# Kernel optimization log

Measured on AMD Instinct MI355X. Metric: run time of the kernel, lower is better.

The kernel has to match this reference:

```python
import jax, jax.numpy as jnp
import numpy as np

IN_FEATURES = 16384
OUT_FEATURES = 16384
NNZ = 1_000_000
BATCH = 256


def setup_inputs() -> dict:
    key = jax.random.key(0)
    k_x, k_w, k_b, k_r, k_c = jax.random.split(key, 5)
    x = jax.random.normal(k_x, (BATCH, IN_FEATURES), dtype=jnp.float32)
    weight_vals = jax.random.normal(k_w, (NNZ,), dtype=jnp.float32)
    bias = jax.random.normal(k_b, (OUT_FEATURES,), dtype=jnp.float32)
    rows = jax.random.randint(k_r, (NNZ,), 0, OUT_FEATURES, dtype=jnp.int32)
    cols = jax.random.randint(k_c, (NNZ,), 0, IN_FEATURES, dtype=jnp.int32)
    return {"x": x, "weight_vals": weight_vals, "bias": bias,
            "rows": rows, "cols": cols}


def reference(x, weight_vals, bias, rows, cols):
    # SparseLinear forward: y = x @ W^T + b, with W sparse COO of shape
    # [out_features, in_features]; (rows, cols) are W's nnz coordinates.
    # Per-edge contribution: x[:, col] * W[row, col], scattered into out[:, row].
    contrib = x[:, cols] * weight_vals  # [B, nnz]
    # segment-sum edges into output features: [nnz, B] -> [out, B]
    out = jax.ops.segment_sum(contrib.T, rows, num_segments=OUT_FEATURES).T
    return out + bias  # [B, out_features]
```

## Files before the change

### kernel.cpp

```cpp
#include <hip/hip_runtime.h>
#include <hip/hip_bf16.h>
#include <hip/hip_fp16.h>

#define BATCH_N 256
#define IN_F    16384
#define OUT_F   16384
#define CAP     128
#define NBUCK   512
#define CAPB    2560
#define EPB     2048
#define TBLK    1024

typedef unsigned int u32x4 __attribute__((ext_vector_type(4)));
typedef float f32x4 __attribute__((ext_vector_type(4)));


__global__ void prep_kernel(const float* __restrict__ x,
                            __hip_bfloat16* __restrict__ xTh,
                            const int* __restrict__ rows,
                            const int* __restrict__ cols,
                            const float* __restrict__ vals, int nnz,
                            int* __restrict__ gcursor,
                            uint2* __restrict__ staging) {
    __shared__ int smem[64 * 65];
    int t = threadIdx.x;
    if (blockIdx.x < TBLK) {
        float* tile = (float*)smem;
        int bid = blockIdx.x;
        int i0 = (bid & 255) * 64;
        int b0 = (bid >> 8) * 64;
        int tx4 = t & 15;
        int r16 = t >> 4;
#pragma unroll
        for (int k = 0; k < 4; ++k) {
            int row = r16 + k * 16;
            f32x4 v = *(const f32x4*)(x + (size_t)(b0 + row) * IN_F + i0 + tx4 * 4);
            tile[row * 65 + tx4 * 4 + 0] = v.x;
            tile[row * 65 + tx4 * 4 + 1] = v.y;
            tile[row * 65 + tx4 * 4 + 2] = v.z;
            tile[row * 65 + tx4 * 4 + 3] = v.w;
        }
        __syncthreads();
        int tx = t & 63, ty = t >> 6;
        int h = b0 >> 7, j0 = b0 & 127;
#pragma unroll
        for (int k = 0; k < 64; k += 4) {
            int col = i0 + ty + k;
            xTh[((size_t)h * IN_F + col) * 128 + j0 + tx] =
                __float2bfloat16(tile[tx * 65 + ty + k]);
        }
    } else {
        int* hist = smem;
        int* base = smem + NBUCK;
        hist[t] = 0; hist[t + 256] = 0;
        __syncthreads();
        int i0 = (blockIdx.x - TBLK) * EPB;
        unsigned int pack[8], vb[8];
        int bk[8];
#pragma unroll
        for (int k = 0; k < 8; ++k) {
            int i = i0 + k * 256 + t;
            if (i < nnz) {
                int r = rows[i], c = cols[i];
                pack[k] = ((unsigned int)r << 14) | (unsigned int)c;
                vb[k] = __float_as_uint(vals[i]);
                bk[k] = r >> 5;
                atomicAdd(&hist[bk[k]], 1);
            } else bk[k] = -1;
        }
        __syncthreads();
#pragma unroll
        for (int q = 0; q < 2; ++q) {
            int bin = t + q * 256;
            int h = hist[bin];
            base[bin] = (h > 0) ? atomicAdd(&gcursor[bin], h) : 0;
        }
        __syncthreads();
        hist[t] = 0; hist[t + 256] = 0;
        __syncthreads();
#pragma unroll
        for (int k = 0; k < 8; ++k) {
            if (bk[k] >= 0) {
                int p = base[bk[k]] + atomicAdd(&hist[bk[k]], 1);
                if (p < CAPB)
                    staging[(size_t)bk[k] * CAPB + p] = make_uint2(pack[k], vb[k]);
            }
        }
    }
}


__global__ void __launch_bounds__(512)
bucket_scatter_kernel(const uint2* __restrict__ staging,
                      const int* __restrict__ gcursor,
                      unsigned int* __restrict__ edges,
                      int* __restrict__ counts) {
    __shared__ int lcnt[32];
    __shared__ unsigned int lbin[32 * CAP];
    int b = blockIdx.x;
    int t = threadIdx.x;
    if (t < 32) lcnt[t] = 0;
    __syncthreads();
    int n = gcursor[b];
    if (n > CAPB) n = CAPB;
    const uint2* st = staging + (size_t)b * CAPB;
    for (int i = t; i < n; i += 512) {
        uint2 rec = __builtin_nontemporal_load((const unsigned long long*)st + i)
                        ? make_uint2(0, 0) : make_uint2(0, 0);
        (void)rec;
        uint2 r2;
        {
            unsigned long long v =
                __builtin_nontemporal_load((const unsigned long long*)st + i);
            r2.x = (unsigned int)(v & 0xffffffffull);
            r2.y = (unsigned int)(v >> 32);
        }
        int rl = (r2.x >> 14) & 31;
        int p = atomicAdd(&lcnt[rl], 1);
        if (p < CAP) {
            unsigned int col = r2.x & 16383u;
            __half hv = __float2half(__uint_as_float(r2.y));
            lbin[rl * CAP + p] = (col << 16) | (unsigned int)__half_as_ushort(hv);
        }
    }
    __syncthreads();
    if (t < 32) {
        int c = lcnt[t];
        if (c > CAP) c = CAP;
        counts[b * 32 + t] = (c + 7) & ~7;
    }
    unsigned int* dst = edges + (size_t)b * 32 * CAP;
    for (int i4 = t; i4 < 32 * CAP / 4; i4 += 512) {
        int i = i4 * 4;
        int row = i >> 7;
        int slot = i & (CAP - 1);
        int c = lcnt[row];
        if (c > CAP) c = CAP;
        int lim = (c + 7) & ~7;
        if (slot < lim) {
            u32x4 v;
            v.x = (slot + 0 < c) ? lbin[i + 0] : 0u;
            v.y = (slot + 1 < c) ? lbin[i + 1] : 0u;
            v.z = (slot + 2 < c) ? lbin[i + 2] : 0u;
            v.w = (slot + 3 < c) ? lbin[i + 3] : 0u;
            __builtin_nontemporal_store(v, (u32x4*)(dst + i));
        }
    }
}


__global__ void accum_kernel(const unsigned int* __restrict__ xh0,
                             const unsigned int* __restrict__ edges,
                             const int*   __restrict__ counts,
                             const float* __restrict__ bias,
                             float* __restrict__ out) {
    __shared__ float slab[128][17];
    int blk = blockIdx.x;
    int h = blk & 1;
    int o0 = (blk >> 1) * 16;
    int w = threadIdx.x >> 6;
    int lane = threadIdx.x & 63;
    const unsigned int* xh = xh0 + (size_t)h * IN_F * 64;
#pragma unroll
    for (int rr = 0; rr < 4; ++rr) {
        int rl = w * 4 + rr;
        int o = __builtin_amdgcn_readfirstlane(o0 + rl);
        int n = counts[o];
        const u32x4* el4 = (const u32x4*)(edges + (size_t)o * CAP);
        float ax = 0.f, ay = 0.f;
        u32x4 ca = el4[0], cb = el4[1];
        for (int j = 0; j < n; j += 8) {
            u32x4 na = el4[(j >> 2) + 2];
            u32x4 nb = el4[(j >> 2) + 3];
            unsigned int e[8];
            e[0] = ca.x; e[1] = ca.y; e[2] = ca.z; e[3] = ca.w;
            e[4] = cb.x; e[5] = cb.y; e[6] = cb.z; e[7] = cb.w;
            unsigned int g[8];
#pragma unroll
            for (int k = 0; k < 8; ++k) {
                const unsigned int* p = xh + ((e[k] >> 16) << 6);
                g[k] = p[lane];
            }
#pragma unroll
            for (int k = 0; k < 8; ++k) {
                float v = __half2float(__ushort_as_half((unsigned short)(e[k] & 0xffffu)));
                ax += __uint_as_float(g[k] << 16) * v;
                ay += __uint_as_float(g[k] & 0xffff0000u) * v;
            }
            ca = na; cb = nb;
        }
        float bv = bias[o];
        slab[2 * lane + 0][rl] = ax + bv;
        slab[2 * lane + 1][rl] = ay + bv;
    }
    __syncthreads();
#pragma unroll
    for (int it = 0; it < 2; ++it) {
        int item = threadIdx.x + it * 256;
        int bl = item >> 2;
        int q = item & 3;
        f32x4 v;
        v.x = slab[bl][q * 4 + 0];
        v.y = slab[bl][q * 4 + 1];
        v.z = slab[bl][q * 4 + 2];
        v.w = slab[bl][q * 4 + 3];
        __builtin_nontemporal_store(v,
            (f32x4*)(out + (size_t)(h * 128 + bl) * OUT_F + o0 + q * 4));
    }
}

extern "C" void kernel_launch(void* const* d_in, const int* in_sizes, int n_in,
                              void* d_out, int out_size, void* d_ws, size_t ws_size,
                              hipStream_t stream) {
    const float* x     = (const float*)d_in[0];
    const float* wvals = (const float*)d_in[1];
    const float* bias  = (const float*)d_in[2];
    const int*   rows  = (const int*)d_in[3];
    const int*   cols  = (const int*)d_in[4];
    float* out = (float*)d_out;
    int nnz = in_sizes[1];

    const size_t MB = 1024 * 1024;
    char* ws = (char*)d_ws;
    __hip_bfloat16* xTh = (__hip_bfloat16*)(ws);
    uint2* staging = (uint2*)(ws + 8 * MB);
    unsigned int* edges = (unsigned int*)(ws + 22 * MB);
    int*   gcursor = (int*)(ws + 30 * MB);
    int*   counts  = (int*)(ws + 30 * MB + 4096);

    (void)hipMemsetAsync(gcursor, 0, NBUCK * sizeof(int), stream);

    int npart = (nnz + EPB - 1) / EPB;
    prep_kernel<<<TBLK + npart, 256, 0, stream>>>(x, xTh, rows, cols, wvals, nnz,
                                                  gcursor, staging);
    bucket_scatter_kernel<<<NBUCK, 512, 0, stream>>>(staging, gcursor, edges, counts);
    accum_kernel<<<(OUT_F / 16) * 2, 256, 0, stream>>>((const unsigned int*)xTh, edges,
                                                       counts, bias, out);
}
```

Before: 141.2 us.

## Scatter edges directly into per-XCD row buckets and drop bucket-scatter kernel

Replaces the two-pass histogram/staging plus bucket-scatter pipeline with a direct per-edge global atomic into per-row cursors. The cursors are partitioned by the XCC ID read from a hardware register, so atomics stay within one die's L2 and do not contend across XCDs. Each record is packed to fp16 value plus column and written straight into a fixed 32-slot sub-bucket per row per XCD. The accumulation kernel then walks the 8 sub-buckets per row. This removes one kernel launch and the staging round trip, but needs a 17 MB memset to zero the padding and adds inner-loop overhead across 8 small sub-lists.

```diff
diff --git a/kernel.cpp b/kernel.cpp
--- a/kernel.cpp
+++ b/kernel.cpp
@@ -5,14 +5,19 @@
 #define BATCH_N 256
 #define IN_F    16384
 #define OUT_F   16384
-#define CAP     128
-#define NBUCK   512
-#define CAPB    2560
+#define NXCD    8
+#define CAPX    32
 #define EPB     2048
 #define TBLK    1024
 
 typedef unsigned int u32x4 __attribute__((ext_vector_type(4)));
 typedef float f32x4 __attribute__((ext_vector_type(4)));
+
+__device__ inline int get_xcc() {
+    unsigned int x;
+    asm volatile("s_getreg_b32 %0, hwreg(HW_REG_XCC_ID)" : "=s"(x));
+    return (int)(x & 7);
+}
 
 
 __global__ void prep_kernel(const float* __restrict__ x,
@@ -20,12 +25,11 @@
                             const int* __restrict__ rows,
                             const int* __restrict__ cols,
                             const float* __restrict__ vals, int nnz,
-                            int* __restrict__ gcursor,
-                            uint2* __restrict__ staging) {
-    __shared__ int smem[64 * 65];
+                            int* __restrict__ cursor,
+                            unsigned int* __restrict__ edges) {
+    __shared__ float tile[64 * 65];
     int t = threadIdx.x;
     if (blockIdx.x < TBLK) {
-        float* tile = (float*)smem;
         int bid = blockIdx.x;
         int i0 = (bid & 255) * 64;
         int b0 = (bid >> 8) * 64;
@@ -50,100 +54,21 @@
                 __float2bfloat16(tile[tx * 65 + ty + k]);
         }
     } else {
-        int* hist = smem;
-        int* base = smem + NBUCK;
-        hist[t] = 0; hist[t + 256] = 0;
-        __syncthreads();
+        int sub = get_xcc();
+        int* cur = cursor + sub * OUT_F;
         int i0 = (blockIdx.x - TBLK) * EPB;
-        unsigned int pack[8], vb[8];
-        int bk[8];
 #pragma unroll
         for (int k = 0; k < 8; ++k) {
             int i = i0 + k * 256 + t;
             if (i < nnz) {
-                int r = rows[i], c = cols[i];
-                pack[k] = ((unsigned int)r << 14) | (unsigned int)c;
-                vb[k] = __float_as_uint(vals[i]);
-                bk[k] = r >> 5;
-                atomicAdd(&hist[bk[k]], 1);
-            } else bk[k] = -1;
-        }
-        __syncthreads();
-#pragma unroll
-        for (int q = 0; q < 2; ++q) {
-            int bin = t + q * 256;
-            int h = hist[bin];
-            base[bin] = (h > 0) ? atomicAdd(&gcursor[bin], h) : 0;
-        }
-        __syncthreads();
-        hist[t] = 0; hist[t + 256] = 0;
-        __syncthreads();
-#pragma unroll
-        for (int k = 0; k < 8; ++k) {
-            if (bk[k] >= 0) {
-                int p = base[bk[k]] + atomicAdd(&hist[bk[k]], 1);
-                if (p < CAPB)
-                    staging[(size_t)bk[k] * CAPB + p] = make_uint2(pack[k], vb[k]);
+                int r = rows[i];
+                unsigned int c = (unsigned int)cols[i];
+                __half hv = __float2half(vals[i]);
+                unsigned int rec = (c << 16) | (unsigned int)__half_as_ushort(hv);
+                int pos = atomicAdd(&cur[r], 1);
+                if (pos < CAPX)
+                    edges[((size_t)r * NXCD + sub) * CAPX + pos] = rec;
             }
-        }
-    }
-}
-
-
-__global__ void __launch_bounds__(512)
-bucket_scatter_kernel(const uint2* __restrict__ staging,
-                      const int* __restrict__ gcursor,
-                      unsigned int* __restrict__ edges,
-                      int* __restrict__ counts) {
-    __shared__ int lcnt[32];
-    __shared__ unsigned int lbin[32 * CAP];
-    int b = blockIdx.x;
-    int t = threadIdx.x;
-    if (t < 32) lcnt[t] = 0;
-    __syncthreads();
-    int n = gcursor[b];
-    if (n > CAPB) n = CAPB;
-    const uint2* st = staging + (size_t)b * CAPB;
-    for (int i = t; i < n; i += 512) {
-        uint2 rec = __builtin_nontemporal_load((const unsigned long long*)st + i)
-                        ? make_uint2(0, 0) : make_uint2(0, 0);
-        (void)rec;
-        uint2 r2;
-        {
-            unsigned long long v =
-                __builtin_nontemporal_load((const unsigned long long*)st + i);
-            r2.x = (unsigned int)(v & 0xffffffffull);
-            r2.y = (unsigned int)(v >> 32);
-        }
-        int rl = (r2.x >> 14) & 31;
-        int p = atomicAdd(&lcnt[rl], 1);
-        if (p < CAP) {
-            unsigned int col = r2.x & 16383u;
-            __half hv = __float2half(__uint_as_float(r2.y));
-            lbin[rl * CAP + p] = (col << 16) | (unsigned int)__half_as_ushort(hv);
-        }
-    }
-    __syncthreads();
-    if (t < 32) {
-        int c = lcnt[t];
-        if (c > CAP) c = CAP;
-        counts[b * 32 + t] = (c + 7) & ~7;
-    }
-    unsigned int* dst = edges + (size_t)b * 32 * CAP;
-    for (int i4 = t; i4 < 32 * CAP / 4; i4 += 512) {
-        int i = i4 * 4;
-        int row = i >> 7;
-        int slot = i & (CAP - 1);
-        int c = lcnt[row];
-        if (c > CAP) c = CAP;
-        int lim = (c + 7) & ~7;
-        if (slot < lim) {
-            u32x4 v;
-            v.x = (slot + 0 < c) ? lbin[i + 0] : 0u;
-            v.y = (slot + 1 < c) ? lbin[i + 1] : 0u;
-            v.z = (slot + 2 < c) ? lbin[i + 2] : 0u;
-            v.w = (slot + 3 < c) ? lbin[i + 3] : 0u;
-            __builtin_nontemporal_store(v, (u32x4*)(dst + i));
         }
     }
 }
@@ -151,7 +76,7 @@
 
 __global__ void accum_kernel(const unsigned int* __restrict__ xh0,
                              const unsigned int* __restrict__ edges,
-                             const int*   __restrict__ counts,
+                             const int*   __restrict__ cursor,
                              const float* __restrict__ bias,
                              float* __restrict__ out) {
     __shared__ float slab[128][17];
@@ -165,29 +90,29 @@
     for (int rr = 0; rr < 4; ++rr) {
         int rl = w * 4 + rr;
         int o = __builtin_amdgcn_readfirstlane(o0 + rl);
-        int n = counts[o];
-        const u32x4* el4 = (const u32x4*)(edges + (size_t)o * CAP);
+        const unsigned int* re = edges + (size_t)o * (NXCD * CAPX);
         float ax = 0.f, ay = 0.f;
-        u32x4 ca = el4[0], cb = el4[1];
-        for (int j = 0; j < n; j += 8) {
-            u32x4 na = el4[(j >> 2) + 2];
-            u32x4 nb = el4[(j >> 2) + 3];
-            unsigned int e[8];
-            e[0] = ca.x; e[1] = ca.y; e[2] = ca.z; e[3] = ca.w;
-            e[4] = cb.x; e[5] = cb.y; e[6] = cb.z; e[7] = cb.w;
-            unsigned int g[8];
+        for (int sub = 0; sub < NXCD; ++sub) {
+            int n = cursor[sub * OUT_F + o];
+            if (n > CAPX) n = CAPX;
+            const unsigned int* el = re + sub * CAPX;
+            for (int j = 0; j < n; j += 8) {
+                unsigned int e[8];
 #pragma unroll
-            for (int k = 0; k < 8; ++k) {
-                const unsigned int* p = xh + ((e[k] >> 16) << 6);
-                g[k] = p[lane];
+                for (int k = 0; k < 8; ++k) e[k] = el[j + k];
+                unsigned int g[8];
+#pragma unroll
+                for (int k = 0; k < 8; ++k) {
+                    const unsigned int* p = xh + ((e[k] >> 16) << 6);
+                    g[k] = p[lane];
+                }
+#pragma unroll
+                for (int k = 0; k < 8; ++k) {
+                    float v = __half2float(__ushort_as_half((unsigned short)(e[k] & 0xffffu)));
+                    ax += __uint_as_float(g[k] << 16) * v;
+                    ay += __uint_as_float(g[k] & 0xffff0000u) * v;
+                }
             }
-#pragma unroll
-            for (int k = 0; k < 8; ++k) {
-                float v = __half2float(__ushort_as_half((unsigned short)(e[k] & 0xffffu)));
-                ax += __uint_as_float(g[k] << 16) * v;
-                ay += __uint_as_float(g[k] & 0xffff0000u) * v;
-            }
-            ca = na; cb = nb;
         }
         float bv = bias[o];
         slab[2 * lane + 0][rl] = ax + bv;
@@ -223,17 +148,14 @@
     const size_t MB = 1024 * 1024;
     char* ws = (char*)d_ws;
     __hip_bfloat16* xTh = (__hip_bfloat16*)(ws);
-    uint2* staging = (uint2*)(ws + 8 * MB);
-    unsigned int* edges = (unsigned int*)(ws + 22 * MB);
-    int*   gcursor = (int*)(ws + 30 * MB);
-    int*   counts  = (int*)(ws + 30 * MB + 4096);
+    int* cursor = (int*)(ws + 8 * MB);
+    unsigned int* edges = (unsigned int*)(ws + 9 * MB);
 
-    (void)hipMemsetAsync(gcursor, 0, NBUCK * sizeof(int), stream);
+    (void)hipMemsetAsync(ws + 8 * MB, 0, 17 * MB, stream);
 
     int npart = (nnz + EPB - 1) / EPB;
     prep_kernel<<<TBLK + npart, 256, 0, stream>>>(x, xTh, rows, cols, wvals, nnz,
-                                                  gcursor, staging);
-    bucket_scatter_kernel<<<NBUCK, 512, 0, stream>>>(staging, gcursor, edges, counts);
+                                                  cursor, edges);
     accum_kernel<<<(OUT_F / 16) * 2, 256, 0, stream>>>((const unsigned int*)xTh, edges,
-                                                       counts, bias, out);
+                                                       cursor, bias, out);
 }
```

Result: slower. 175.8 us (+24.6%).
